# Kernel tuning notes

Hardware: AMD Instinct MI355X
Metric: run time of the kernel (lower is better)

## Reference

```python
import jax, jax.numpy as jnp
import numpy as np

N = 50000      # nodes
E = 800000     # edges (before self-loops)
DIN = 128      # in_channels
DH = 64        # hidden_channels
HEADS = 2
DOUT = 64      # out_channels
NEG_SLOPE = 0.2  # PyG GATConv leaky_relu slope


def setup_inputs() -> dict:
    key = jax.random.key(0)
    ks = jax.random.split(key, 10)
    node_emb = jax.random.normal(ks[0], (N, DIN), dtype=jnp.float32)
    edge_index = jax.random.randint(ks[1], (2, E), 0, N, dtype=jnp.int64)
    # conv1: in -> hidden, heads=2, concat=True
    W1 = jax.random.normal(ks[2], (DIN, HEADS * DH), dtype=jnp.float32) / np.sqrt(DIN)
    att_src1 = jax.random.normal(ks[3], (HEADS, DH), dtype=jnp.float32) * 0.1
    att_dst1 = jax.random.normal(ks[4], (HEADS, DH), dtype=jnp.float32) * 0.1
    b1 = jnp.zeros((HEADS * DH,), dtype=jnp.float32)
    # conv2: hidden*heads -> out, heads=1, concat=False
    W2 = jax.random.normal(ks[5], (HEADS * DH, 1 * DOUT), dtype=jnp.float32) / np.sqrt(HEADS * DH)
    att_src2 = jax.random.normal(ks[6], (1, DOUT), dtype=jnp.float32) * 0.1
    att_dst2 = jax.random.normal(ks[7], (1, DOUT), dtype=jnp.float32) * 0.1
    b2 = jnp.zeros((DOUT,), dtype=jnp.float32)
    return {"node_emb": node_emb, "edge_index": edge_index,
            "W1": W1, "att_src1": att_src1, "att_dst1": att_dst1, "b1": b1,
            "W2": W2, "att_src2": att_src2, "att_dst2": att_dst2, "b2": b2}


def gat_layer(x, src, dst, W, att_src, att_dst, bias, heads, concat, n):
    # x: [N, Fin]; W: [Fin, heads*C]; att_*: [heads, C]
    C = W.shape[1] // heads
    h = (x @ W).reshape(n, heads, C)                       # [N, H, C]
    a_src = jnp.einsum('nhc,hc->nh', h, att_src)           # [N, H]
    a_dst = jnp.einsum('nhc,hc->nh', h, att_dst)           # [N, H]
    e = jax.nn.leaky_relu(a_src[src] + a_dst[dst], NEG_SLOPE)  # [E, H]
    # segment softmax over incoming edges of each destination node
    m = jax.ops.segment_max(e, dst, num_segments=n)        # [N, H]
    ex = jnp.exp(e - m[dst])
    denom = jax.ops.segment_sum(ex, dst, num_segments=n)   # [N, H]
    alpha = ex / denom[dst]                                # [E, H]
    out = jax.ops.segment_sum(h[src] * alpha[:, :, None], dst, num_segments=n)  # [N, H, C]
    if concat:
        out = out.reshape(n, heads * C)
    else:
        out = out.mean(axis=1)
    return out + bias


def reference(node_emb, edge_index, W1, att_src1, att_dst1, b1, W2, att_src2, att_dst2, b2):
    loops = jnp.arange(N, dtype=edge_index.dtype)
    src = jnp.concatenate([edge_index[0], loops])  # PyG add_self_loops=True
    dst = jnp.concatenate([edge_index[1], loops])
    h = gat_layer(node_emb, src, dst, W1, att_src1, att_dst1, b1, HEADS, True, N)
    h = jax.nn.elu(h)
    # dropout is identity in eval mode
    out = gat_layer(h, src, dst, W2, att_src2, att_dst2, b2, 1, False, N)
    return out
```

## Files before the change

kernel.cpp:

```cpp
#include <hip/hip_runtime.h>
#include <hip/hip_fp16.h>
#include <math.h>

constexpr float NEG_SLOPE = 0.2f;
constexpr int NPART = 8;
constexpr int WSLOT = 16;

__device__ inline __half2 u2h(unsigned int u) { return *reinterpret_cast<__half2*>(&u); }
__device__ inline unsigned int h2u(__half2 h) { return *reinterpret_cast<unsigned int*>(&h); }

__device__ inline void fmamix8(uint4 v, float al, float* acc) {
    float2 f0 = __half22float2(u2h(v.x)), f1 = __half22float2(u2h(v.y));
    float2 f2 = __half22float2(u2h(v.z)), f3 = __half22float2(u2h(v.w));
    acc[0] = fmaf(al, f0.x, acc[0]); acc[1] = fmaf(al, f0.y, acc[1]);
    acc[2] = fmaf(al, f1.x, acc[2]); acc[3] = fmaf(al, f1.y, acc[3]);
    acc[4] = fmaf(al, f2.x, acc[4]); acc[5] = fmaf(al, f2.y, acc[5]);
    acc[6] = fmaf(al, f3.x, acc[6]); acc[7] = fmaf(al, f3.y, acc[7]);
}

__device__ inline int ell_resolve(const unsigned short* __restrict__ ell,
                                  const int* pre, int node, int l) {
    int p = 0;
#pragma unroll
    for (int t = 1; t < NPART; t++)
        if (l >= pre[t]) p = t;
    int slot = l - pre[p];
    return (int)ell[((size_t)node * NPART + p) * WSLOT + slot];
}

__global__ __launch_bounds__(256) void k_fused1(
    const int* __restrict__ src, const int* __restrict__ dst, int e, int S, int G,
    int* __restrict__ cur, unsigned short* __restrict__ ell,
    const float* __restrict__ x, const float* __restrict__ W,
    const float* __restrict__ a_src, const float* __restrict__ a_dst,
    __half* __restrict__ h1h, float* __restrict__ att, int n) {
    __shared__ float xs[32 * 128];
    __shared__ __half wsh[64 * 128];
    int bid = blockIdx.x;
    int t = threadIdx.x;

    int third = bid / 3;
    bool interleave = (2 * S <= G + 2);
    bool isScat = interleave ? ((bid % 3 == 0) && (third < S)) : (bid < S);
    if (isScat) {
        int sid = interleave ? third : bid;
        int p = bid & (NPART - 1);
        int i0 = (sid * 256 + t) * 4;
        if (i0 + 3 < e) {
            int4 d4 = *reinterpret_cast<const int4*>(dst + i0);
            int4 s4 = *reinterpret_cast<const int4*>(src + i0);
            int a0 = atomicAdd(&cur[d4.x * NPART + p], 1);
            int a1 = atomicAdd(&cur[d4.y * NPART + p], 1);
            int a2 = atomicAdd(&cur[d4.z * NPART + p], 1);
            int a3 = atomicAdd(&cur[d4.w * NPART + p], 1);
            if (a0 < WSLOT) ell[((size_t)d4.x * NPART + p) * WSLOT + a0] = (unsigned short)s4.x;
            if (a1 < WSLOT) ell[((size_t)d4.y * NPART + p) * WSLOT + a1] = (unsigned short)s4.y;
            if (a2 < WSLOT) ell[((size_t)d4.z * NPART + p) * WSLOT + a2] = (unsigned short)s4.z;
            if (a3 < WSLOT) ell[((size_t)d4.w * NPART + p) * WSLOT + a3] = (unsigned short)s4.w;
        } else {
            for (int i = i0; i < e; i++) {
                int d = dst[i];
                int slot = atomicAdd(&cur[d * NPART + p], 1);
                if (slot < WSLOT) ell[((size_t)d * NPART + p) * WSLOT + slot] = (unsigned short)src[i];
            }
        }
        return;
    }
    int gid = interleave ? (bid - min(S, (bid + 2) / 3)) : (bid - S);
    if (gid >= G) return;

    int row0 = gid * 32;
    const float4* xv = (const float4*)x;
    float4* xsv = (float4*)xs;
#pragma unroll
    for (int ii = 0; ii < 4; ii++) {
        int i = t + 256 * ii;
        int r = i >> 5, c4 = i & 31;
        int gr = row0 + r;
        float4 v = (gr < n) ? xv[(size_t)gr * 32 + c4] : make_float4(0.f, 0.f, 0.f, 0.f);
        xsv[i] = v;
    }

    int tc = t & 31;
    int tr = t >> 5;
    float acc[4][4];
#pragma unroll
    for (int i = 0; i < 4; i++)
#pragma unroll
        for (int j = 0; j < 4; j++) acc[i][j] = 0.f;

    const float4* Wv = (const float4*)W;
    uint2* wsv = (uint2*)wsh;
    const uint2* wsv2 = (const uint2*)wsh;
#pragma unroll
    for (int kh = 0; kh < 2; kh++) {
        __syncthreads();
#pragma unroll
        for (int ii = 0; ii < 8; ii++) {
            int i = t + 256 * ii;
            float4 w = Wv[kh * 2048 + i];
            __half2 a = __floats2half2_rn(w.x, w.y);
            __half2 b = __floats2half2_rn(w.z, w.w);
            uint2 o; o.x = h2u(a); o.y = h2u(b);
            wsv[i] = o;
        }
        __syncthreads();
        for (int kk = 0; kk < 64; kk++) {
            uint2 wu = wsv2[kk * 32 + tc];
            float2 wA = __half22float2(u2h(wu.x));
            float2 wB = __half22float2(u2h(wu.y));
#pragma unroll
            for (int i = 0; i < 4; i++) {
                float xvv = xs[(tr * 4 + i) * 128 + kh * 64 + kk];
                acc[i][0] = fmaf(xvv, wA.x, acc[i][0]);
                acc[i][1] = fmaf(xvv, wA.y, acc[i][1]);
                acc[i][2] = fmaf(xvv, wB.x, acc[i][2]);
                acc[i][3] = fmaf(xvv, wB.y, acc[i][3]);
            }
        }
    }

#pragma unroll
    for (int i = 0; i < 4; i++) {
        int gr = row0 + tr * 4 + i;
        if (gr < n) {
            __half2 p01 = __floats2half2_rn(acc[i][0], acc[i][1]);
            __half2 p23 = __floats2half2_rn(acc[i][2], acc[i][3]);
            uint2 o; o.x = h2u(p01); o.y = h2u(p23);
            *reinterpret_cast<uint2*>(h1h + (size_t)gr * 128 + 4 * tc) = o;
        }
    }
    const float4* asv = (const float4*)a_src;
    const float4* adv = (const float4*)a_dst;
    float4 as4 = asv[tc], ad4 = adv[tc];
    int lane = t & 63;
#pragma unroll
    for (int i = 0; i < 4; i++) {
        float s = acc[i][0] * as4.x + acc[i][1] * as4.y + acc[i][2] * as4.z + acc[i][3] * as4.w;
        float d = acc[i][0] * ad4.x + acc[i][1] * ad4.y + acc[i][2] * ad4.z + acc[i][3] * ad4.w;
#pragma unroll
        for (int o = 1; o < 16; o <<= 1) {
            s += __shfl_xor(s, o);
            d += __shfl_xor(d, o);
        }
        float s1 = __shfl(s, (lane & 32) + 16);
        float d1 = __shfl(d, (lane & 32) + 16);
        int gr = row0 + tr * 4 + i;
        if ((lane & 31) == 0 && gr < n) {
            ((float4*)att)[gr] = make_float4(s, s1, d, d1);
        }
    }
}

__global__ __launch_bounds__(256) void k_gemm2(const __half* __restrict__ x2h,
                                               const float* __restrict__ W,
                                               const float* __restrict__ a_src,
                                               const float* __restrict__ a_dst,
                                               __half* __restrict__ h2h,
                                               float* __restrict__ att, int n) {
    __shared__ float xs[32 * 128];
    __shared__ __half wsh[128 * 64];
    int t = threadIdx.x;
    const float4* Wv = (const float4*)W;
    uint2* wsv = (uint2*)wsh;
#pragma unroll
    for (int i = 0; i < 8; i++) {
        float4 w = Wv[t + 256 * i];
        __half2 a = __floats2half2_rn(w.x, w.y);
        __half2 b = __floats2half2_rn(w.z, w.w);
        uint2 o; o.x = h2u(a); o.y = h2u(b);
        wsv[t + 256 * i] = o;
    }
    int row0 = blockIdx.x * 32;
    const uint2* xv = (const uint2*)x2h;
    float4* xsv = (float4*)xs;
#pragma unroll
    for (int ii = 0; ii < 4; ii++) {
        int i = t + 256 * ii;
        int r = i >> 5, c4 = i & 31;
        int gr = row0 + r;
        uint2 u = (gr < n) ? xv[(size_t)gr * 32 + c4] : make_uint2(0u, 0u);
        float2 lo = __half22float2(u2h(u.x)), hi = __half22float2(u2h(u.y));
        xsv[i] = make_float4(lo.x, lo.y, hi.x, hi.y);
    }
    __syncthreads();
    int tc = t & 15;
    int tr = t >> 4;
    float acc[2][4];
#pragma unroll
    for (int i = 0; i < 2; i++)
#pragma unroll
        for (int j = 0; j < 4; j++) acc[i][j] = 0.f;
    const uint2* wsv2 = (const uint2*)wsh;
    for (int k = 0; k < 128; k++) {
        uint2 wu = wsv2[k * 16 + tc];
        float2 wA = __half22float2(u2h(wu.x));
        float2 wB = __half22float2(u2h(wu.y));
#pragma unroll
        for (int i = 0; i < 2; i++) {
            float xvv = xs[(tr * 2 + i) * 128 + k];
            acc[i][0] = fmaf(xvv, wA.x, acc[i][0]);
            acc[i][1] = fmaf(xvv, wA.y, acc[i][1]);
            acc[i][2] = fmaf(xvv, wB.x, acc[i][2]);
            acc[i][3] = fmaf(xvv, wB.y, acc[i][3]);
        }
    }
#pragma unroll
    for (int i = 0; i < 2; i++) {
        int gr = row0 + tr * 2 + i;
        if (gr < n) {
            __half2 p01 = __floats2half2_rn(acc[i][0], acc[i][1]);
            __half2 p23 = __floats2half2_rn(acc[i][2], acc[i][3]);
            uint2 o; o.x = h2u(p01); o.y = h2u(p23);
            *reinterpret_cast<uint2*>(h2h + (size_t)gr * 64 + 4 * tc) = o;
        }
    }
    const float4* asv = (const float4*)a_src;
    const float4* adv = (const float4*)a_dst;
    float4 as4 = asv[tc], ad4 = adv[tc];
#pragma unroll
    for (int i = 0; i < 2; i++) {
        float s = acc[i][0] * as4.x + acc[i][1] * as4.y + acc[i][2] * as4.z + acc[i][3] * as4.w;
        float d = acc[i][0] * ad4.x + acc[i][1] * ad4.y + acc[i][2] * ad4.z + acc[i][3] * ad4.w;
#pragma unroll
        for (int o = 1; o < 16; o <<= 1) {
            s += __shfl_xor(s, o);
            d += __shfl_xor(d, o);
        }
        int gr = row0 + tr * 2 + i;
        if (tc == 0 && gr < n) {
            ((float2*)att)[gr] = make_float2(s, d);
        }
    }
}

__global__ __launch_bounds__(256) void k_aggr1(const int* __restrict__ cur,
                                               const unsigned short* __restrict__ ell,
                                               const float* __restrict__ att,
                                               const __half* __restrict__ h1h,
                                               const float* __restrict__ bias,
                                               __half* __restrict__ x2h, int n) {
    int wid = threadIdx.x >> 6, lane = threadIdx.x & 63;
    int node = blockIdx.x * 4 + wid;
    if (node >= n) return;

    int cnt = 0;
    if (lane < NPART) cnt = cur[node * NPART + lane];
    int pre[NPART];
    int tot = 1;
#pragma unroll
    for (int p = 0; p < NPART; p++) {
        int cc = __shfl(cnt, p);
        cc = cc < WSLOT ? cc : WSLOT;
        pre[p] = tot;
        tot += cc;
    }

    const float4* attv = (const float4*)att;
    float4 an = attv[node];
    float ad0 = an.z, ad1 = an.w;

    int chq = lane & 15;
    int g = lane >> 4;
    bool hsel = (chq >= 8);

    float f[8];

    if (tot <= 64) {
        int c = node;
        float p0 = 0.f, p1 = 0.f;
        if (lane < tot) {
            if (lane > 0) c = ell_resolve(ell, pre, node, lane);
            float4 a = attv[c];
            float e0 = a.x + ad0; e0 = e0 > 0.f ? e0 : NEG_SLOPE * e0;
            float e1 = a.y + ad1; e1 = e1 > 0.f ? e1 : NEG_SLOPE * e1;
            p0 = __expf(e0); p1 = __expf(e1);
        }
        float sum0 = p0, sum1 = p1;
#pragma unroll
        for (int d = 1; d < 64; d <<= 1) {
            sum0 += __shfl_xor(sum0, d);
            sum1 += __shfl_xor(sum1, d);
        }
        float rsel = hsel ? (1.f / sum1) : (1.f / sum0);

        __half2 z = __float2half2_rn(0.f);
        __half2 hacc0 = z, hacc1 = z, hacc2 = z, hacc3 = z;
        for (int k0 = 0; k0 < tot; k0 += 32) {
            uint4 v[8];
            __half2 al2[8];
#pragma unroll
            for (int u = 0; u < 8; u++) {
                int k = k0 + 4 * u + g;
                int ks = k & 63;
                int sn = __shfl(c, ks);
                float pa = __shfl(p0, ks);
                float pb = __shfl(p1, ks);
                float alf = (k < tot) ? (hsel ? pb : pa) * rsel : 0.f;
                al2[u] = __float2half2_rn(alf);
                v[u] = *reinterpret_cast<const uint4*>(h1h + (size_t)sn * 128 + 8 * chq);
            }
#pragma unroll
            for (int u = 0; u < 8; u++) {
                hacc0 = __hfma2(al2[u], u2h(v[u].x), hacc0);
                hacc1 = __hfma2(al2[u], u2h(v[u].y), hacc1);
                hacc2 = __hfma2(al2[u], u2h(v[u].z), hacc2);
                hacc3 = __hfma2(al2[u], u2h(v[u].w), hacc3);
            }
        }
        f[0] = __low2float(hacc0); f[1] = __high2float(hacc0);
        f[2] = __low2float(hacc1); f[3] = __high2float(hacc1);
        f[4] = __low2float(hacc2); f[5] = __high2float(hacc2);
        f[6] = __low2float(hacc3); f[7] = __high2float(hacc3);
    } else {
        float sum0 = 0.f, sum1 = 0.f;
        for (int l = lane; l < tot; l += 64) {
            int c = (l == 0) ? node : ell_resolve(ell, pre, node, l);
            float4 a = attv[c];
            float e0 = a.x + ad0; e0 = e0 > 0.f ? e0 : NEG_SLOPE * e0;
            float e1 = a.y + ad1; e1 = e1 > 0.f ? e1 : NEG_SLOPE * e1;
            sum0 += __expf(e0); sum1 += __expf(e1);
        }
#pragma unroll
        for (int d = 1; d < 64; d <<= 1) {
            sum0 += __shfl_xor(sum0, d);
            sum1 += __shfl_xor(sum1, d);
        }
        float rsel = hsel ? (1.f / sum1) : (1.f / sum0);
        float acc[8];
#pragma unroll
        for (int i = 0; i < 8; i++) acc[i] = 0.f;
        for (int j = 0; j < tot; j += 4) {
            int l = j + g;
            bool valid = (l < tot);
            int lc = valid ? l : 0;
            int sn = (lc == 0) ? node : ell_resolve(ell, pre, node, lc);
            float4 a = attv[sn];
            float e0 = a.x + ad0; e0 = e0 > 0.f ? e0 : NEG_SLOPE * e0;
            float e1 = a.y + ad1; e1 = e1 > 0.f ? e1 : NEG_SLOPE * e1;
            float pp = hsel ? __expf(e1) : __expf(e0);
            float al = valid ? pp * rsel : 0.f;
            uint4 v = *reinterpret_cast<const uint4*>(h1h + (size_t)sn * 128 + 8 * chq);
            fmamix8(v, al, acc);
        }
#pragma unroll
        for (int i = 0; i < 8; i++) f[i] = acc[i];
    }

#pragma unroll
    for (int i = 0; i < 8; i++) {
        f[i] += __shfl_xor(f[i], 16);
        f[i] += __shfl_xor(f[i], 32);
    }
    if (lane < 16) {
        const float4* bv = (const float4*)bias;
        float4 bA = bv[2 * chq], bB = bv[2 * chq + 1];
        float o[8];
        o[0] = f[0] + bA.x; o[1] = f[1] + bA.y;
        o[2] = f[2] + bA.z; o[3] = f[3] + bA.w;
        o[4] = f[4] + bB.x; o[5] = f[5] + bB.y;
        o[6] = f[6] + bB.z; o[7] = f[7] + bB.w;
#pragma unroll
        for (int i = 0; i < 8; i++) o[i] = o[i] > 0.f ? o[i] : (__expf(o[i]) - 1.f);
        __half2 q01 = __floats2half2_rn(o[0], o[1]);
        __half2 q23 = __floats2half2_rn(o[2], o[3]);
        __half2 q45 = __floats2half2_rn(o[4], o[5]);
        __half2 q67 = __floats2half2_rn(o[6], o[7]);
        uint4 w; w.x = h2u(q01); w.y = h2u(q23); w.z = h2u(q45); w.w = h2u(q67);
        *reinterpret_cast<uint4*>(x2h + (size_t)node * 128 + 8 * chq) = w;
    }
}

__global__ __launch_bounds__(256) void k_aggr2(const int* __restrict__ cur,
                                               const unsigned short* __restrict__ ell,
                                               const float* __restrict__ att,
                                               const __half* __restrict__ h2h,
                                               const float* __restrict__ bias,
                                               float* __restrict__ out, int n) {
    int wid = threadIdx.x >> 6, lane = threadIdx.x & 63;
    int node = blockIdx.x * 4 + wid;
    if (node >= n) return;

    int cnt = 0;
    if (lane < NPART) cnt = cur[node * NPART + lane];
    int pre[NPART];
    int tot = 1;
#pragma unroll
    for (int p = 0; p < NPART; p++) {
        int cc = __shfl(cnt, p);
        cc = cc < WSLOT ? cc : WSLOT;
        pre[p] = tot;
        tot += cc;
    }

    const float2* attv = (const float2*)att;
    float adn = attv[node].y;
    int chq = lane & 7;
    int g = lane >> 3;

    float f[8];

    if (tot <= 64) {
        int c = node;
        float p = 0.f;
        if (lane < tot) {
            if (lane > 0) c = ell_resolve(ell, pre, node, lane);
            float e = attv[c].x + adn;
            e = e > 0.f ? e : NEG_SLOPE * e;
            p = __expf(e);
        }
        float sum = p;
#pragma unroll
        for (int d = 1; d < 64; d <<= 1) sum += __shfl_xor(sum, d);
        float r = 1.f / sum;

        __half2 z = __float2half2_rn(0.f);
        __half2 hacc0 = z, hacc1 = z, hacc2 = z, hacc3 = z;
        for (int k0 = 0; k0 < tot; k0 += 32) {
            uint4 v[4];
            __half2 al2[4];
#pragma unroll
            for (int u = 0; u < 4; u++) {
                int k = k0 + 8 * u + g;
                int ks = k & 63;
                int sn = __shfl(c, ks);
                float pk = __shfl(p, ks);
                float alf = (k < tot) ? pk * r : 0.f;
                al2[u] = __float2half2_rn(alf);
                v[u] = *reinterpret_cast<const uint4*>(h2h + (size_t)sn * 64 + 8 * chq);
            }
#pragma unroll
            for (int u = 0; u < 4; u++) {
                hacc0 = __hfma2(al2[u], u2h(v[u].x), hacc0);
                hacc1 = __hfma2(al2[u], u2h(v[u].y), hacc1);
                hacc2 = __hfma2(al2[u], u2h(v[u].z), hacc2);
                hacc3 = __hfma2(al2[u], u2h(v[u].w), hacc3);
            }
        }
        f[0] = __low2float(hacc0); f[1] = __high2float(hacc0);
        f[2] = __low2float(hacc1); f[3] = __high2float(hacc1);
        f[4] = __low2float(hacc2); f[5] = __high2float(hacc2);
        f[6] = __low2float(hacc3); f[7] = __high2float(hacc3);
    } else {
        float sum = 0.f;
        for (int l = lane; l < tot; l += 64) {
            int c = (l == 0) ? node : ell_resolve(ell, pre, node, l);
            float e = attv[c].x + adn;
            e = e > 0.f ? e : NEG_SLOPE * e;
            sum += __expf(e);
        }
#pragma unroll
        for (int d = 1; d < 64; d <<= 1) sum += __shfl_xor(sum, d);
        float r = 1.f / sum;
        float acc[8];
#pragma unroll
        for (int i = 0; i < 8; i++) acc[i] = 0.f;
        for (int j = 0; j < tot; j += 8) {
            int l = j + g;
            bool valid = (l < tot);
            int lc = valid ? l : 0;
            int sn = (lc == 0) ? node : ell_resolve(ell, pre, node, lc);
            float e = attv[sn].x + adn;
            e = e > 0.f ? e : NEG_SLOPE * e;
            float al = valid ? __expf(e) * r : 0.f;
            uint4 v = *reinterpret_cast<const uint4*>(h2h + (size_t)sn * 64 + 8 * chq);
            fmamix8(v, al, acc);
        }
#pragma unroll
        for (int i = 0; i < 8; i++) f[i] = acc[i];
    }

#pragma unroll
    for (int i = 0; i < 8; i++) {
        f[i] += __shfl_xor(f[i], 8);
        f[i] += __shfl_xor(f[i], 16);
        f[i] += __shfl_xor(f[i], 32);
    }
    if (lane < 8) {
        const float4* bv = (const float4*)bias;
        float4 bA = bv[2 * chq], bB = bv[2 * chq + 1];
        float4* ov = (float4*)(out + (size_t)node * 64 + 8 * chq);
        ov[0] = make_float4(f[0] + bA.x, f[1] + bA.y, f[2] + bA.z, f[3] + bA.w);
        ov[1] = make_float4(f[4] + bB.x, f[5] + bB.y, f[6] + bB.z, f[7] + bB.w);
    }
}

extern "C" void kernel_launch(void* const* d_in, const int* in_sizes, int n_in,
                              void* d_out, int out_size, void* d_ws, size_t ws_size,
                              hipStream_t stream) {
    const float* x    = (const float*)d_in[0];
    const int*   ei   = (const int*)d_in[1];
    const float* W1   = (const float*)d_in[2];
    const float* asr1 = (const float*)d_in[3];
    const float* adt1 = (const float*)d_in[4];
    const float* b1   = (const float*)d_in[5];
    const float* W2   = (const float*)d_in[6];
    const float* asr2 = (const float*)d_in[7];
    const float* adt2 = (const float*)d_in[8];
    const float* b2   = (const float*)d_in[9];
    float* out = (float*)d_out;

    const int N = in_sizes[0] / 128;
    const int E = in_sizes[1] / 2;
    const int* srcI = ei;
    const int* dstI = ei + E;

    char* p = (char*)d_ws;
    auto alloc = [&](size_t b) -> void* {
        void* r = (void*)p;
        p += ((b + 255) / 256) * 256;
        return r;
    };
    int* cur = (int*)alloc(sizeof(int) * (size_t)NPART * N);
    unsigned short* ell = (unsigned short*)alloc(sizeof(unsigned short) *
                                                 (size_t)NPART * N * WSLOT);
    __half* h1h = (__half*)alloc(sizeof(__half) * (size_t)N * 128);
    float* att1 = (float*)alloc(sizeof(float) * (size_t)N * 4);
    __half* x2h = (__half*)alloc(sizeof(__half) * (size_t)N * 128);
    __half* h2h = (__half*)alloc(sizeof(__half) * (size_t)N * 64);
    float* att2 = (float*)alloc(sizeof(float) * (size_t)N * 2);

    int S = (E + 1023) / 1024;
    int G = (N + 31) / 32;
    int nbNode4 = (N + 3) / 4;
    int nbRow32 = (N + 31) / 32;

    hipMemsetAsync(cur, 0, sizeof(int) * (size_t)NPART * N, stream);

    k_fused1<<<S + G, 256, 0, stream>>>(srcI, dstI, E, S, G, cur, ell,
                                        x, W1, asr1, adt1, h1h, att1, N);

    k_aggr1<<<nbNode4, 256, 0, stream>>>(cur, ell, att1, h1h, b1, x2h, N);

    k_gemm2<<<nbRow32, 256, 0, stream>>>(x2h, W2, asr2, adt2, h2h, att2, N);
    k_aggr2<<<nbNode4, 256, 0, stream>>>(cur, ell, att2, h2h, b2, out, N);
}
```

Baseline: 142.3 us.

## Fuse layer-2 GEMM and attention logits into layer-1 aggregation kernel

```diff
diff --git a/kernel.cpp b/kernel.cpp
--- a/kernel.cpp
+++ b/kernel.cpp
@@ -8,6 +8,12 @@
 
 __device__ inline __half2 u2h(unsigned int u) { return *reinterpret_cast<__half2*>(&u); }
 __device__ inline unsigned int h2u(__half2 h) { return *reinterpret_cast<unsigned int*>(&h); }
+
+#if __has_builtin(__builtin_amdgcn_readlane)
+#define RDLANE(v, l) __builtin_amdgcn_readlane((v), (l))
+#else
+#define RDLANE(v, l) __shfl((v), (l))
+#endif
 
 __device__ inline void fmamix8(uint4 v, float al, float* acc) {
     float2 f0 = __half22float2(u2h(v.x)), f1 = __half22float2(u2h(v.y));
@@ -26,6 +32,14 @@
         if (l >= pre[t]) p = t;
     int slot = l - pre[p];
     return (int)ell[((size_t)node * NPART + p) * WSLOT + slot];
+}
+
+__global__ void k_wt2(const float* __restrict__ W2, __half* __restrict__ Wt2h) {
+    int id = blockIdx.x * 256 + threadIdx.x;
+    if (id < 64 * 128) {
+        int c = id >> 7, k = id & 127;
+        Wt2h[id] = __float2half(W2[k * 64 + c]);
+    }
 }
 
 __global__ __launch_bounds__(256) void k_fused1(
@@ -152,94 +166,12 @@
     }
 }
 
-__global__ __launch_bounds__(256) void k_gemm2(const __half* __restrict__ x2h,
-                                               const float* __restrict__ W,
-                                               const float* __restrict__ a_src,
-                                               const float* __restrict__ a_dst,
-                                               __half* __restrict__ h2h,
-                                               float* __restrict__ att, int n) {
-    __shared__ float xs[32 * 128];
-    __shared__ __half wsh[128 * 64];
-    int t = threadIdx.x;
-    const float4* Wv = (const float4*)W;
-    uint2* wsv = (uint2*)wsh;
-#pragma unroll
-    for (int i = 0; i < 8; i++) {
-        float4 w = Wv[t + 256 * i];
-        __half2 a = __floats2half2_rn(w.x, w.y);
-        __half2 b = __floats2half2_rn(w.z, w.w);
-        uint2 o; o.x = h2u(a); o.y = h2u(b);
-        wsv[t + 256 * i] = o;
-    }
-    int row0 = blockIdx.x * 32;
-    const uint2* xv = (const uint2*)x2h;
-    float4* xsv = (float4*)xs;
-#pragma unroll
-    for (int ii = 0; ii < 4; ii++) {
-        int i = t + 256 * ii;
-        int r = i >> 5, c4 = i & 31;
-        int gr = row0 + r;
-        uint2 u = (gr < n) ? xv[(size_t)gr * 32 + c4] : make_uint2(0u, 0u);
-        float2 lo = __half22float2(u2h(u.x)), hi = __half22float2(u2h(u.y));
-        xsv[i] = make_float4(lo.x, lo.y, hi.x, hi.y);
-    }
-    __syncthreads();
-    int tc = t & 15;
-    int tr = t >> 4;
-    float acc[2][4];
-#pragma unroll
-    for (int i = 0; i < 2; i++)
-#pragma unroll
-        for (int j = 0; j < 4; j++) acc[i][j] = 0.f;
-    const uint2* wsv2 = (const uint2*)wsh;
-    for (int k = 0; k < 128; k++) {
-        uint2 wu = wsv2[k * 16 + tc];
-        float2 wA = __half22float2(u2h(wu.x));
-        float2 wB = __half22float2(u2h(wu.y));
-#pragma unroll
-        for (int i = 0; i < 2; i++) {
-            float xvv = xs[(tr * 2 + i) * 128 + k];
-            acc[i][0] = fmaf(xvv, wA.x, acc[i][0]);
-            acc[i][1] = fmaf(xvv, wA.y, acc[i][1]);
-            acc[i][2] = fmaf(xvv, wB.x, acc[i][2]);
-            acc[i][3] = fmaf(xvv, wB.y, acc[i][3]);
-        }
-    }
-#pragma unroll
-    for (int i = 0; i < 2; i++) {
-        int gr = row0 + tr * 2 + i;
-        if (gr < n) {
-            __half2 p01 = __floats2half2_rn(acc[i][0], acc[i][1]);
-            __half2 p23 = __floats2half2_rn(acc[i][2], acc[i][3]);
-            uint2 o; o.x = h2u(p01); o.y = h2u(p23);
-            *reinterpret_cast<uint2*>(h2h + (size_t)gr * 64 + 4 * tc) = o;
-        }
-    }
-    const float4* asv = (const float4*)a_src;
-    const float4* adv = (const float4*)a_dst;
-    float4 as4 = asv[tc], ad4 = adv[tc];
-#pragma unroll
-    for (int i = 0; i < 2; i++) {
-        float s = acc[i][0] * as4.x + acc[i][1] * as4.y + acc[i][2] * as4.z + acc[i][3] * as4.w;
-        float d = acc[i][0] * ad4.x + acc[i][1] * ad4.y + acc[i][2] * ad4.z + acc[i][3] * ad4.w;
-#pragma unroll
-        for (int o = 1; o < 16; o <<= 1) {
-            s += __shfl_xor(s, o);
-            d += __shfl_xor(d, o);
-        }
-        int gr = row0 + tr * 2 + i;
-        if (tc == 0 && gr < n) {
-            ((float2*)att)[gr] = make_float2(s, d);
-        }
-    }
-}
-
-__global__ __launch_bounds__(256) void k_aggr1(const int* __restrict__ cur,
-                                               const unsigned short* __restrict__ ell,
-                                               const float* __restrict__ att,
-                                               const __half* __restrict__ h1h,
-                                               const float* __restrict__ bias,
-                                               __half* __restrict__ x2h, int n) {
+__global__ __launch_bounds__(256, 4) void k_aggr1g2(
+    const int* __restrict__ cur, const unsigned short* __restrict__ ell,
+    const float* __restrict__ att, const __half* __restrict__ h1h,
+    const float* __restrict__ bias, const __half* __restrict__ Wt2h,
+    const float* __restrict__ as2, const float* __restrict__ ad2,
+    __half* __restrict__ h2h, float* __restrict__ att2, int n) {
     int wid = threadIdx.x >> 6, lane = threadIdx.x & 63;
     int node = blockIdx.x * 4 + wid;
     if (node >= n) return;
@@ -352,23 +284,53 @@
         f[i] += __shfl_xor(f[i], 16);
         f[i] += __shfl_xor(f[i], 32);
     }
-    if (lane < 16) {
-        const float4* bv = (const float4*)bias;
-        float4 bA = bv[2 * chq], bB = bv[2 * chq + 1];
-        float o[8];
-        o[0] = f[0] + bA.x; o[1] = f[1] + bA.y;
-        o[2] = f[2] + bA.z; o[3] = f[3] + bA.w;
-        o[4] = f[4] + bB.x; o[5] = f[5] + bB.y;
-        o[6] = f[6] + bB.z; o[7] = f[7] + bB.w;
-#pragma unroll
-        for (int i = 0; i < 8; i++) o[i] = o[i] > 0.f ? o[i] : (__expf(o[i]) - 1.f);
-        __half2 q01 = __floats2half2_rn(o[0], o[1]);
-        __half2 q23 = __floats2half2_rn(o[2], o[3]);
-        __half2 q45 = __floats2half2_rn(o[4], o[5]);
-        __half2 q67 = __floats2half2_rn(o[6], o[7]);
-        uint4 w; w.x = h2u(q01); w.y = h2u(q23); w.z = h2u(q45); w.w = h2u(q67);
-        *reinterpret_cast<uint4*>(x2h + (size_t)node * 128 + 8 * chq) = w;
-    }
+
+    const float4* bv = (const float4*)bias;
+    float4 bA = bv[2 * chq], bB = bv[2 * chq + 1];
+    float o[8];
+    o[0] = f[0] + bA.x; o[1] = f[1] + bA.y;
+    o[2] = f[2] + bA.z; o[3] = f[3] + bA.w;
+    o[4] = f[4] + bB.x; o[5] = f[5] + bB.y;
+    o[6] = f[6] + bB.z; o[7] = f[7] + bB.w;
+#pragma unroll
+    for (int i = 0; i < 8; i++) o[i] = o[i] > 0.f ? o[i] : (__expf(o[i]) - 1.f);
+
+    float h2c = 0.f;
+    const uint4* wcol = reinterpret_cast<const uint4*>(Wt2h + (size_t)lane * 128);
+#pragma unroll
+    for (int h = 0; h < 2; h++) {
+        uint4 wv[8];
+#pragma unroll
+        for (int m = 0; m < 8; m++) wv[m] = wcol[h * 8 + m];
+#pragma unroll
+        for (int m = 0; m < 8; m++) {
+            int q = h * 8 + m;
+            float xk[8];
+#pragma unroll
+            for (int j = 0; j < 8; j++)
+                xk[j] = __int_as_float(RDLANE(__float_as_int(o[j]), q));
+            __half2 w01 = u2h(wv[m].x), w23 = u2h(wv[m].y);
+            __half2 w45 = u2h(wv[m].z), w67 = u2h(wv[m].w);
+            h2c = fmaf(xk[0], __low2float(w01), h2c);
+            h2c = fmaf(xk[1], __high2float(w01), h2c);
+            h2c = fmaf(xk[2], __low2float(w23), h2c);
+            h2c = fmaf(xk[3], __high2float(w23), h2c);
+            h2c = fmaf(xk[4], __low2float(w45), h2c);
+            h2c = fmaf(xk[5], __high2float(w45), h2c);
+            h2c = fmaf(xk[6], __low2float(w67), h2c);
+            h2c = fmaf(xk[7], __high2float(w67), h2c);
+        }
+    }
+    h2h[(size_t)node * 64 + lane] = __float2half(h2c);
+
+    float s2 = h2c * as2[lane];
+    float d2 = h2c * ad2[lane];
+#pragma unroll
+    for (int off = 1; off < 64; off <<= 1) {
+        s2 += __shfl_xor(s2, off);
+        d2 += __shfl_xor(d2, off);
+    }
+    if (lane == 0) ((float2*)att2)[node] = make_float2(s2, d2);
 }
 
 __global__ __launch_bounds__(256) void k_aggr2(const int* __restrict__ cur,
@@ -516,22 +478,23 @@
                                                  (size_t)NPART * N * WSLOT);
     __half* h1h = (__half*)alloc(sizeof(__half) * (size_t)N * 128);
     float* att1 = (float*)alloc(sizeof(float) * (size_t)N * 4);
-    __half* x2h = (__half*)alloc(sizeof(__half) * (size_t)N * 128);
     __half* h2h = (__half*)alloc(sizeof(__half) * (size_t)N * 64);
     float* att2 = (float*)alloc(sizeof(float) * (size_t)N * 2);
+    __half* Wt2h = (__half*)alloc(sizeof(__half) * 64 * 128);
 
     int S = (E + 1023) / 1024;
     int G = (N + 31) / 32;
     int nbNode4 = (N + 3) / 4;
-    int nbRow32 = (N + 31) / 32;
 
     hipMemsetAsync(cur, 0, sizeof(int) * (size_t)NPART * N, stream);
+
+    k_wt2<<<32, 256, 0, stream>>>(W2, Wt2h);
 
     k_fused1<<<S + G, 256, 0, stream>>>(srcI, dstI, E, S, G, cur, ell,
                                         x, W1, asr1, adt1, h1h, att1, N);
 
-    k_aggr1<<<nbNode4, 256, 0, stream>>>(cur, ell, att1, h1h, b1, x2h, N);
-
-    k_gemm2<<<nbRow32, 256, 0, stream>>>(x2h, W2, asr2, adt2, h2h, att2, N);
+    k_aggr1g2<<<nbNode4, 256, 0, stream>>>(cur, ell, att1, h1h, b1, Wt2h,
+                                           asr2, adt2, h2h, att2, N);
+
     k_aggr2<<<nbNode4, 256, 0, stream>>>(cur, ell, att2, h2h, b2, out, N);
 }
```

Result: slower. 196.5 us (+38.1%).
